# Performance work log

Measured on AMD Instinct MI355X. Metric: run time of the kernel, lower is better.

Reference implementation:

```python
import jax, jax.numpy as jnp
import numpy as np

N_HEADS = 16
D_EMBED = 1024
N_CROSS = 768
D_HEAD = D_EMBED // N_HEADS


def setup_inputs() -> dict:
    key = jax.random.key(0)
    ks = jax.random.split(key, 10)
    B, S = 2, 2048
    x = jax.random.normal(ks[0], (B, S, D_EMBED), dtype=jnp.float32)
    context = jax.random.normal(ks[1], (B, S, N_CROSS), dtype=jnp.float32)
    sq = 1.0 / np.sqrt(D_EMBED)
    sc = 1.0 / np.sqrt(N_CROSS)
    Wq = jax.random.normal(ks[2], (D_EMBED, D_EMBED), dtype=jnp.float32) * sq
    bq = jnp.zeros((D_EMBED,), dtype=jnp.float32)
    Wk = jax.random.normal(ks[3], (N_CROSS, D_EMBED), dtype=jnp.float32) * sc
    bk = jnp.zeros((D_EMBED,), dtype=jnp.float32)
    Wv = jax.random.normal(ks[4], (N_CROSS, D_EMBED), dtype=jnp.float32) * sc
    bv = jnp.zeros((D_EMBED,), dtype=jnp.float32)
    Wo = jax.random.normal(ks[5], (D_EMBED, D_EMBED), dtype=jnp.float32) * sq
    bo = jnp.zeros((D_EMBED,), dtype=jnp.float32)
    return {"x": x, "context": context, "Wq": Wq, "bq": bq, "Wk": Wk, "bk": bk,
            "Wv": Wv, "bv": bv, "Wo": Wo, "bo": bo}


def reference(x, context, Wq, bq, Wk, bk, Wv, bv, Wo, bo):
    B, S, _ = x.shape

    def split_heads(t):  # [B,S,E] -> [B,H,S,Dh]
        return t.reshape(B, S, N_HEADS, D_HEAD).transpose(0, 2, 1, 3)

    q = split_heads(x @ Wq + bq)
    k = split_heads(context @ Wk + bk)
    v = split_heads(context @ Wv + bv)

    scale = 1.0 / np.sqrt(D_HEAD)
    scores = jnp.einsum('bhqd,bhkd->bhqk', q, k) * scale
    attn = jax.nn.softmax(scores, axis=-1)
    out = jnp.einsum('bhqk,bhkd->bhqd', attn, v)
    out = out.transpose(0, 2, 1, 3).reshape(B, S, D_EMBED)
    return out @ Wo + bo
```

## Files before the change

### kernel.cpp

```cpp
#include <hip/hip_runtime.h>
#include <math.h>


namespace {

typedef short bfr __attribute__((ext_vector_type(8)));
typedef short s4v __attribute__((ext_vector_type(4)));
typedef unsigned u4v __attribute__((ext_vector_type(4)));
typedef float accf __attribute__((ext_vector_type(16)));

#define MFMA32(a, b, c) __builtin_amdgcn_mfma_f32_32x32x16_bf16(a, b, c, 0, 0, 0)

__device__ inline short f2bf(float f) {
    unsigned u = __float_as_uint(f);
    u += 0x7fffu + ((u >> 16) & 1u);
    return (short)(u >> 16);
}
__device__ inline float bf2f(short s) {
    return __uint_as_float(((unsigned)(unsigned short)s) << 16);
}
__device__ inline float fexp2(float x) { return __builtin_amdgcn_exp2f(x); }
__device__ inline accf zero16() {
    accf z;
#pragma unroll
    for (int i = 0; i < 16; ++i) z[i] = 0.f;
    return z;
}
__device__ inline void dma16(const void* g, void* l) {
    __builtin_amdgcn_global_load_lds(
        (const __attribute__((address_space(1))) void*)g,
        (__attribute__((address_space(3))) void*)l, 16, 0, 0);
}

__global__ __launch_bounds__(256) void prep(
    const float* __restrict__ x, const float* __restrict__ ctx,
    short* __restrict__ xb, short* __restrict__ cb,
    const float* __restrict__ Wq, const float* __restrict__ Wk,
    const float* __restrict__ Wv, const float* __restrict__ Wo,
    short* __restrict__ Wqt, short* __restrict__ Wkt,
    short* __restrict__ Wvt, short* __restrict__ Wot) {
    __shared__ short t[64][68];
    const int bx = blockIdx.x;
    if (bx < 7168) {
        int i = bx * 256 + threadIdx.x;
        if (i < 1048576) {
            float4 v = ((const float4*)x)[i];
            s4v p = {f2bf(v.x), f2bf(v.y), f2bf(v.z), f2bf(v.w)};
            ((s4v*)xb)[i] = p;
        } else {
            int j = i - 1048576;
            float4 v = ((const float4*)ctx)[j];
            s4v p = {f2bf(v.x), f2bf(v.y), f2bf(v.z), f2bf(v.w)};
            ((s4v*)cb)[j] = p;
        }
        return;
    }
    const int idx = bx - 7168;
    const int z = idx >> 8, gy = (idx >> 4) & 15, gx = idx & 15;
    const float* W;
    short* Wt;
    int K;
    switch (z) {
        case 0: W = Wq; Wt = Wqt; K = 1024; break;
        case 1: W = Wk; Wt = Wkt; K = 768; break;
        case 2: W = Wv; Wt = Wvt; K = 768; break;
        default: W = Wo; Wt = Wot; K = 1024; break;
    }
    const int k0 = gy * 64;
    if (k0 >= K) return;
    const int tid = threadIdx.x;
    const int n0 = gx * 64;
    const int kr = tid >> 4, nc = (tid & 15) * 4;
#pragma unroll
    for (int rep = 0; rep < 4; ++rep) {
        int k = kr + rep * 16;
        float4 v = *(const float4*)&W[(size_t)(k0 + k) * 1024 + n0 + nc];
        t[nc + 0][k] = f2bf(v.x);
        t[nc + 1][k] = f2bf(v.y);
        t[nc + 2][k] = f2bf(v.z);
        t[nc + 3][k] = f2bf(v.w);
    }
    __syncthreads();
    const int nr = tid >> 4, kc = (tid & 15) * 4;
#pragma unroll
    for (int rep = 0; rep < 4; ++rep) {
        int n = nr + rep * 16;
        s4v p = {t[n][kc], t[n][kc + 1], t[n][kc + 2], t[n][kc + 3]};
        *(s4v*)&Wt[(size_t)(n0 + n) * K + k0 + kc] = p;
    }
}

__global__ __launch_bounds__(512, 6) void gemm_qkv(
    const short* __restrict__ xb, const short* __restrict__ cb,
    const short* __restrict__ Wqt, const short* __restrict__ Wkt,
    const short* __restrict__ Wvt, const float* __restrict__ bq,
    const float* __restrict__ bk, const float* __restrict__ bv,
    short* __restrict__ Qf, short* __restrict__ Kf, short* __restrict__ Vt,
    float qscale) {
    const int bid = blockIdx.x;
    const int z = bid >> 8;
    const int local = bid & 255;
    const short* A  = (z == 0) ? xb : cb;
    const short* Bt = (z == 0) ? Wqt : ((z == 1) ? Wkt : Wvt);
    const float* bias = (z == 0) ? bq : ((z == 1) ? bk : bv);
    const int K = (z == 0) ? 1024 : 768;
    const int NIT = K / 32;
    const float scale = (z == 0) ? qscale : 1.f;
    short* out = (z == 0) ? Qf : ((z == 1) ? Kf : Vt);

    __shared__ short As[12288];
    __shared__ short Bs[12288];
    const int t = threadIdx.x, lane = t & 63, w = t >> 6;
    const int lm = lane & 31, h2 = lane >> 5;
    const int wm = w & 1, wn = w >> 1;
    const int m0 = (local & 31) * 128, n0 = (local >> 5) * 128;

    const int st = t ^ ((t >> 3) & 7);
    const int srow = st >> 2, scol = (st & 3) * 8;
    const short* ga = A + (size_t)(m0 + srow) * K + scol;
    const short* gb = Bt + (size_t)(n0 + srow) * K + scol;

    const int xorv = (lm >> 1) & 7;
    const int rA0 = wm * 64 + lm, rB0 = wn * 32 + lm;

    accf acc[2] = {zero16(), zero16()};

    dma16(ga, &As[w * 512]);
    dma16(gb, &Bs[w * 512]);
    __builtin_amdgcn_sched_barrier(0);
    dma16(ga + 32, &As[4096 + w * 512]);
    dma16(gb + 32, &Bs[4096 + w * 512]);
    __builtin_amdgcn_sched_barrier(0);

    int buf = 0;
#pragma unroll 1
    for (int it = 0; it < NIT; ++it) {
        __builtin_amdgcn_sched_barrier(0);
        asm volatile("s_waitcnt vmcnt(2)" ::: "memory");
        __builtin_amdgcn_s_barrier();
        __builtin_amdgcn_sched_barrier(0);
        {
            const int nx = (it + 2 >= NIT) ? (it + 2 - NIT) : (it + 2);
            const int nb = (buf + 2 >= 3) ? (buf - 1) : (buf + 2);
            dma16(ga + nx * 32, &As[nb * 4096 + w * 512]);
            dma16(gb + nx * 32, &Bs[nb * 4096 + w * 512]);
        }
        const short* bA = &As[buf * 4096];
        const short* bB = &Bs[buf * 4096];
#pragma unroll
        for (int kk8 = 0; kk8 < 4; kk8 += 2) {
            bfr a0 = *(const bfr*)&bA[((rA0 * 4 + h2 + kk8) ^ xorv) * 8];
            bfr a1 = *(const bfr*)&bA[(((rA0 + 32) * 4 + h2 + kk8) ^ xorv) * 8];
            bfr b0 = *(const bfr*)&bB[((rB0 * 4 + h2 + kk8) ^ xorv) * 8];
            acc[0] = MFMA32(a0, b0, acc[0]);
            acc[1] = MFMA32(a1, b0, acc[1]);
        }
        buf = (buf + 1 == 3) ? 0 : buf + 1;
    }
    asm volatile("s_waitcnt vmcnt(0)" ::: "memory");
    __builtin_amdgcn_sched_barrier(0);

    const int n = n0 + wn * 32 + lm;
    const float bn = bias[n];
    const int hh = n >> 6, dd = n & 63;
#pragma unroll
    for (int mt = 0; mt < 2; ++mt) {
        const int mbase = m0 + wm * 64 + mt * 32 + 4 * h2;
        if (z != 2) {
            const int cb2 = (dd >> 4) * 512 + ((dd >> 3) & 1) * 256 + (dd & 7);
#pragma unroll
            for (int r = 0; r < 16; ++r) {
                const int m = mbase + (r & 3) + 8 * (r >> 2);
                const int bb = m >> 11, q = m & 2047;
                float v = (acc[mt][r] + bn) * scale;
                out[((size_t)((bb * 16 + hh) * 64 + (q >> 5))) * 2048 +
                    cb2 + (q & 31) * 8] = f2bf(v);
            }
        } else {
            const int dblk = dd >> 5, lmv = dd & 31;
#pragma unroll
            for (int g = 0; g < 4; ++g) {
                const int m = mbase + 8 * g;
                const int bb = m >> 11, s = m & 2047;
                const int kvt = s >> 6, kc = (s >> 4) & 3;
                const int h2v = (s >> 3) & 1, j0 = s & 7;
                s4v pq = {f2bf(acc[mt][4 * g + 0] + bn),
                          f2bf(acc[mt][4 * g + 1] + bn),
                          f2bf(acc[mt][4 * g + 2] + bn),
                          f2bf(acc[mt][4 * g + 3] + bn)};
                *(s4v*)(out +
                        ((size_t)(((bb * 16 + hh) * 32 + kvt) * 2 + dblk)) * 2048 +
                        kc * 512 + h2v * 256 + lmv * 8 + j0) = pq;
            }
        }
    }
}

__global__ __launch_bounds__(512) void gemm_out(
    const short* __restrict__ p0, const short* __restrict__ p1,
    const float* __restrict__ lsum, const short* __restrict__ Bt,
    const float* __restrict__ bias, float* __restrict__ out) {
    constexpr int K = 1024, NIT = 32;
    __shared__ short As[8192];
    __shared__ short Bs[8192];
    const int t = threadIdx.x, lane = t & 63, w = t >> 6;
    const int lm = lane & 31, h2 = lane >> 5;
    const int wm = w & 1, wn = w >> 1;
    const int bid = blockIdx.x;
    const int m0 = (bid & 31) * 128, n0 = (bid >> 5) * 128;

    const int st = t ^ ((t >> 3) & 7);
    const int srow = st >> 2, scol = (st & 3) * 8;
    const int gm = m0 + srow;
    const int b = gm >> 11, q = gm & 2047;
    const short* pa0 = p0 + (size_t)gm * 1024 + scol;
    const short* pa1 = p1 + (size_t)gm * 1024 + scol;
    const short* gb = Bt + (size_t)(n0 + srow) * K + scol;

    float inv[16];
#pragma unroll
    for (int h = 0; h < 16; ++h) {
        float l0 = lsum[((size_t)b * 16 + h) * 2048 + q];
        float l1 = lsum[((size_t)(2 + b) * 16 + h) * 2048 + q];
        inv[h] = 1.f / (l0 + l1);
    }

    const int xorv = (lm >> 1) & 7;
    const int rA0 = wm * 64 + lm, rB0 = wn * 32 + lm;

    accf acc[2] = {zero16(), zero16()};

    dma16(gb, &Bs[w * 512]);
    {
        bfr v0 = *(const bfr*)pa0;
        bfr v1 = *(const bfr*)pa1;
        const float iv = inv[0];
        bfr pk;
#pragma unroll
        for (int j = 0; j < 8; ++j)
            pk[j] = f2bf((bf2f(v0[j]) + bf2f(v1[j])) * iv);
        *(bfr*)&As[t * 8] = pk;
    }

#pragma unroll 1
    for (int it = 0; it < NIT; ++it) {
        const int p = it & 1;
        __syncthreads();
        bfr v0, v1;
        const bool nxt = (it + 1 < NIT);
        if (nxt) {
            const int ktn = (it + 1) * 32;
            dma16(gb + ktn, &Bs[(1 - p) * 4096 + w * 512]);
            v0 = *(const bfr*)(pa0 + ktn);
            v1 = *(const bfr*)(pa1 + ktn);
        }
        const short* bA = &As[p * 4096];
        const short* bB = &Bs[p * 4096];
#pragma unroll
        for (int kk8 = 0; kk8 < 4; kk8 += 2) {
            bfr a0 = *(const bfr*)&bA[((rA0 * 4 + h2 + kk8) ^ xorv) * 8];
            bfr a1 = *(const bfr*)&bA[(((rA0 + 32) * 4 + h2 + kk8) ^ xorv) * 8];
            bfr b0 = *(const bfr*)&bB[((rB0 * 4 + h2 + kk8) ^ xorv) * 8];
            acc[0] = MFMA32(a0, b0, acc[0]);
            acc[1] = MFMA32(a1, b0, acc[1]);
        }
        if (nxt) {
            const float iv = inv[(it + 1) >> 1];
            bfr pk;
#pragma unroll
            for (int j = 0; j < 8; ++j)
                pk[j] = f2bf((bf2f(v0[j]) + bf2f(v1[j])) * iv);
            *(bfr*)&As[(1 - p) * 4096 + t * 8] = pk;
        }
    }

    const int n = n0 + wn * 32 + lm;
    const float bn = bias[n];
#pragma unroll
    for (int mt = 0; mt < 2; ++mt) {
        const int mbase = m0 + wm * 64 + mt * 32 + 4 * h2;
#pragma unroll
        for (int r = 0; r < 16; ++r) {
            const int m = mbase + (r & 3) + 8 * (r >> 2);
            out[(size_t)m * 1024 + n] = acc[mt][r] + bn;
        }
    }
}

__global__ __launch_bounds__(256, 3) void attn(
    const short* __restrict__ Qf, const short* __restrict__ Kf,
    const short* __restrict__ Vt, short* __restrict__ part,
    float* __restrict__ lsum) {
    __shared__ short smem[16384];
    const int bid = blockIdx.x;
    const int hidx = bid & 31, qs = bid >> 5;
    const int split = qs & 1, qb = qs >> 1;
    const int b = hidx >> 4, h = hidx & 15;
    const int lane = threadIdx.x & 63, wv = threadIdx.x >> 6;
    const int lm = lane & 31, h2 = lane >> 5;
    const bool hb = h2 != 0;
    const int q0 = qb * 128 + wv * 32;

    const short* qbase =
        Qf + ((size_t)(hidx * 64 + (q0 >> 5))) * 2048 + lane * 8;
    bfr qf[4];
#pragma unroll
    for (int kc = 0; kc < 4; ++kc) qf[kc] = *(const bfr*)(qbase + kc * 512);

    const short* khead = Kf + (size_t)hidx * 131072 + split * 65536;
    const short* vhead = Vt + (size_t)hidx * 131072 + split * 65536;
    const short* gsrc =
        ((wv < 2) ? (khead + wv * 2048) : (vhead + (wv - 2) * 2048)) + lane * 8;

#pragma unroll
    for (int i = 0; i < 4; ++i)
        dma16(gsrc + i * 512, &smem[wv * 2048 + i * 512]);

    accf oa0 = zero16(), oa1 = zero16();
    float la0 = 0.f, la1 = 0.f;

#pragma unroll 1
    for (int it = 0; it < 16; ++it) {
        const int p = it & 1;
        __syncthreads();
        if (it + 1 < 16) {
            const short* gn = gsrc + (size_t)(it + 1) * 4096;
            short* ln = &smem[(1 - p) * 8192 + wv * 2048];
#pragma unroll
            for (int i = 0; i < 4; ++i) dma16(gn + i * 512, ln + i * 512);
        }
        const short* kb = &smem[p * 8192];
        bfr kf0[4], kf1[4], vf0[4], vf1[4];
#pragma unroll
        for (int kc = 0; kc < 4; ++kc) {
            kf0[kc] = *(const bfr*)&kb[kc * 512 + lane * 8];
            kf1[kc] = *(const bfr*)&kb[2048 + kc * 512 + lane * 8];
            vf0[kc] = *(const bfr*)&kb[4096 + kc * 512 + lane * 8];
            vf1[kc] = *(const bfr*)&kb[6144 + kc * 512 + lane * 8];
        }
        accf s0 = zero16(), s1 = zero16();
#pragma unroll
        for (int kc = 0; kc < 4; ++kc) {
            s0 = MFMA32(kf0[kc], qf[kc], s0);
            s1 = MFMA32(kf1[kc], qf[kc], s1);
        }

#pragma unroll
        for (int i = 0; i < 16; ++i) s0[i] = fexp2(s0[i]);
#pragma unroll
        for (int i = 0; i < 16; ++i) s1[i] = fexp2(s1[i]);
#pragma unroll
        for (int i = 0; i < 16; ++i) {
            if (i & 1) la1 += s0[i] + s1[i];
            else       la0 += s0[i] + s1[i];
        }

        bfr pb[4];
#pragma unroll
        for (int kc = 0; kc < 4; ++kc) {
            const accf& s = (kc < 2) ? s0 : s1;
            const int base = 8 * (kc & 1);
            unsigned Lw0 = __builtin_amdgcn_perm(__float_as_uint(s[base + 1]),
                                                 __float_as_uint(s[base + 0]),
                                                 0x07060302u);
            unsigned Lw1 = __builtin_amdgcn_perm(__float_as_uint(s[base + 3]),
                                                 __float_as_uint(s[base + 2]),
                                                 0x07060302u);
            unsigned Hw0 = __builtin_amdgcn_perm(__float_as_uint(s[base + 5]),
                                                 __float_as_uint(s[base + 4]),
                                                 0x07060302u);
            unsigned Hw1 = __builtin_amdgcn_perm(__float_as_uint(s[base + 7]),
                                                 __float_as_uint(s[base + 6]),
                                                 0x07060302u);
            unsigned c0 = hb ? Lw0 : Hw0;
            unsigned c1 = hb ? Lw1 : Hw1;
            unsigned r0 = (unsigned)__shfl_xor((int)c0, 32);
            unsigned r1 = (unsigned)__shfl_xor((int)c1, 32);
            u4v pw = {hb ? r0 : Lw0, hb ? r1 : Lw1,
                      hb ? Hw0 : r0, hb ? Hw1 : r1};
            pb[kc] = __builtin_bit_cast(bfr, pw);
        }

#pragma unroll
        for (int kc = 0; kc < 4; ++kc) {
            oa0 = MFMA32(vf0[kc], pb[kc], oa0);
            oa1 = MFMA32(vf1[kc], pb[kc], oa1);
        }
    }

    float ls = la0 + la1;
    ls += __shfl_xor(ls, 32);
    if (!hb) lsum[((size_t)(split * 2 + b) * 16 + h) * 2048 + q0 + lm] = ls;

    short* orow = part + (size_t)split * 4194304 +
                  (size_t)(b * 2048 + q0 + lm) * 1024 + h * 64;
#pragma unroll
    for (int dt = 0; dt < 2; ++dt) {
        const accf& oa = dt ? oa1 : oa0;
#pragma unroll
        for (int g = 0; g < 4; ++g) {
            const int d0 = dt * 32 + 4 * h2 + 8 * g;
            s4v p = {f2bf(oa[4 * g + 0]), f2bf(oa[4 * g + 1]),
                     f2bf(oa[4 * g + 2]), f2bf(oa[4 * g + 3])};
            *(s4v*)(orow + d0) = p;
        }
    }
}

}

extern "C" void kernel_launch(void* const* d_in, const int* in_sizes, int n_in,
                              void* d_out, int out_size, void* d_ws,
                              size_t ws_size, hipStream_t stream) {
    const float* x   = (const float*)d_in[0];
    const float* ctx = (const float*)d_in[1];
    const float* Wq  = (const float*)d_in[2];
    const float* bq  = (const float*)d_in[3];
    const float* Wk  = (const float*)d_in[4];
    const float* bk  = (const float*)d_in[5];
    const float* Wv  = (const float*)d_in[6];
    const float* bv  = (const float*)d_in[7];
    const float* Wo  = (const float*)d_in[8];
    const float* bo  = (const float*)d_in[9];

    short* xb  = (short*)d_ws;
    short* cb  = xb + (size_t)4096 * 1024;
    short* Wqt = cb + (size_t)4096 * 768;
    short* Wkt = Wqt + (size_t)1024 * 1024;
    short* Wvt = Wkt + (size_t)1024 * 768;
    short* Wot = Wvt + (size_t)1024 * 768;
    short* Qf  = Wot + (size_t)1024 * 1024;
    short* Kf  = Qf + (size_t)4096 * 1024;
    short* Vt  = Kf + (size_t)4096 * 1024;
    short* p0  = Vt + (size_t)4096 * 1024;
    short* p1  = p0 + (size_t)4096 * 1024;
    float* lsum = (float*)(p1 + (size_t)4096 * 1024);

    prep<<<8192, 256, 0, stream>>>(x, ctx, xb, cb, Wq, Wk, Wv, Wo,
                                   Wqt, Wkt, Wvt, Wot);

    const float qscale = 0.125f * 1.44269504088896f;
    gemm_qkv<<<768, 512, 0, stream>>>(xb, cb, Wqt, Wkt, Wvt,
                                      bq, bk, bv, Qf, Kf, Vt, qscale);

    attn<<<1024, 256, 0, stream>>>(Qf, Kf, Vt, p0, lsum);

    gemm_out<<<256, 512, 0, stream>>>(p0, p1, lsum, Wot, bo, (float*)d_out);
}
```

Baseline: 208.2 us.

## Split split-KV combine into separate kernel and triple-buffer DMA output GEMM

The normalisation and merge of the two split-KV attention partials moves out of the output-projection GEMM into a standalone elementwise kernel that writes the normalised bf16 result back into p0. The output GEMM then loads both A and B tiles by direct DMA into a three-stage shared-memory ring, waiting with explicit vmcnt and barriers instead of doing register-side conversion in the loop. This aims to hide global latency better in the GEMM, at the cost of an extra kernel launch and an extra read/write pass over the 8MB partial buffer. Past the end of K, the prefetch wraps around and loads redundant tiles.

```diff
diff --git a/kernel.cpp b/kernel.cpp
--- a/kernel.cpp
+++ b/kernel.cpp
@@ -196,13 +196,32 @@
     }
 }
 
-__global__ __launch_bounds__(512) void gemm_out(
-    const short* __restrict__ p0, const short* __restrict__ p1,
-    const float* __restrict__ lsum, const short* __restrict__ Bt,
+__global__ __launch_bounds__(256) void combine(
+    short* __restrict__ p0, const short* __restrict__ p1,
+    const float* __restrict__ lsum) {
+    const int i = blockIdx.x * 256 + threadIdx.x;
+    const size_t gi = (size_t)i * 8;
+    const int row = (int)(gi >> 10), col = (int)(gi & 1023);
+    const int h = col >> 6;
+    const int b = row >> 11, q = row & 2047;
+    const float l0 = lsum[((size_t)b * 16 + h) * 2048 + q];
+    const float l1 = lsum[((size_t)(2 + b) * 16 + h) * 2048 + q];
+    const float iv = 1.f / (l0 + l1);
+    bfr v0 = *(const bfr*)(p0 + gi);
+    bfr v1 = *(const bfr*)(p1 + gi);
+    bfr pk;
+#pragma unroll
+    for (int j = 0; j < 8; ++j)
+        pk[j] = f2bf((bf2f(v0[j]) + bf2f(v1[j])) * iv);
+    *(bfr*)(p0 + gi) = pk;
+}
+
+__global__ __launch_bounds__(512, 6) void gemm_o(
+    const short* __restrict__ Af, const short* __restrict__ Bt,
     const float* __restrict__ bias, float* __restrict__ out) {
     constexpr int K = 1024, NIT = 32;
-    __shared__ short As[8192];
-    __shared__ short Bs[8192];
+    __shared__ short As[12288];
+    __shared__ short Bs[12288];
     const int t = threadIdx.x, lane = t & 63, w = t >> 6;
     const int lm = lane & 31, h2 = lane >> 5;
     const int wm = w & 1, wn = w >> 1;
@@ -211,51 +230,36 @@
 
     const int st = t ^ ((t >> 3) & 7);
     const int srow = st >> 2, scol = (st & 3) * 8;
-    const int gm = m0 + srow;
-    const int b = gm >> 11, q = gm & 2047;
-    const short* pa0 = p0 + (size_t)gm * 1024 + scol;
-    const short* pa1 = p1 + (size_t)gm * 1024 + scol;
+    const short* ga = Af + (size_t)(m0 + srow) * K + scol;
     const short* gb = Bt + (size_t)(n0 + srow) * K + scol;
-
-    float inv[16];
-#pragma unroll
-    for (int h = 0; h < 16; ++h) {
-        float l0 = lsum[((size_t)b * 16 + h) * 2048 + q];
-        float l1 = lsum[((size_t)(2 + b) * 16 + h) * 2048 + q];
-        inv[h] = 1.f / (l0 + l1);
-    }
 
     const int xorv = (lm >> 1) & 7;
     const int rA0 = wm * 64 + lm, rB0 = wn * 32 + lm;
 
     accf acc[2] = {zero16(), zero16()};
 
+    dma16(ga, &As[w * 512]);
     dma16(gb, &Bs[w * 512]);
-    {
-        bfr v0 = *(const bfr*)pa0;
-        bfr v1 = *(const bfr*)pa1;
-        const float iv = inv[0];
-        bfr pk;
-#pragma unroll
-        for (int j = 0; j < 8; ++j)
-            pk[j] = f2bf((bf2f(v0[j]) + bf2f(v1[j])) * iv);
-        *(bfr*)&As[t * 8] = pk;
-    }
-
+    __builtin_amdgcn_sched_barrier(0);
+    dma16(ga + 32, &As[4096 + w * 512]);
+    dma16(gb + 32, &Bs[4096 + w * 512]);
+    __builtin_amdgcn_sched_barrier(0);
+
+    int buf = 0;
 #pragma unroll 1
     for (int it = 0; it < NIT; ++it) {
-        const int p = it & 1;
-        __syncthreads();
-        bfr v0, v1;
-        const bool nxt = (it + 1 < NIT);
-        if (nxt) {
-            const int ktn = (it + 1) * 32;
-            dma16(gb + ktn, &Bs[(1 - p) * 4096 + w * 512]);
-            v0 = *(const bfr*)(pa0 + ktn);
-            v1 = *(const bfr*)(pa1 + ktn);
-        }
-        const short* bA = &As[p * 4096];
-        const short* bB = &Bs[p * 4096];
+        __builtin_amdgcn_sched_barrier(0);
+        asm volatile("s_waitcnt vmcnt(2)" ::: "memory");
+        __builtin_amdgcn_s_barrier();
+        __builtin_amdgcn_sched_barrier(0);
+        {
+            const int nx = (it + 2 >= NIT) ? (it + 2 - NIT) : (it + 2);
+            const int nb = (buf + 2 >= 3) ? (buf - 1) : (buf + 2);
+            dma16(ga + nx * 32, &As[nb * 4096 + w * 512]);
+            dma16(gb + nx * 32, &Bs[nb * 4096 + w * 512]);
+        }
+        const short* bA = &As[buf * 4096];
+        const short* bB = &Bs[buf * 4096];
 #pragma unroll
         for (int kk8 = 0; kk8 < 4; kk8 += 2) {
             bfr a0 = *(const bfr*)&bA[((rA0 * 4 + h2 + kk8) ^ xorv) * 8];
@@ -264,15 +268,10 @@
             acc[0] = MFMA32(a0, b0, acc[0]);
             acc[1] = MFMA32(a1, b0, acc[1]);
         }
-        if (nxt) {
-            const float iv = inv[(it + 1) >> 1];
-            bfr pk;
-#pragma unroll
-            for (int j = 0; j < 8; ++j)
-                pk[j] = f2bf((bf2f(v0[j]) + bf2f(v1[j])) * iv);
-            *(bfr*)&As[(1 - p) * 4096 + t * 8] = pk;
-        }
-    }
+        buf = (buf + 1 == 3) ? 0 : buf + 1;
+    }
+    asm volatile("s_waitcnt vmcnt(0)" ::: "memory");
+    __builtin_amdgcn_sched_barrier(0);
 
     const int n = n0 + wn * 32 + lm;
     const float bn = bias[n];
@@ -445,5 +444,7 @@
 
     attn<<<1024, 256, 0, stream>>>(Qf, Kf, Vt, p0, lsum);
 
-    gemm_out<<<256, 512, 0, stream>>>(p0, p1, lsum, Wot, bo, (float*)d_out);
-}
+    combine<<<2048, 256, 0, stream>>>(p0, p1, lsum);
+
+    gemm_o<<<256, 512, 0, stream>>>(p0, Wot, bo, (float*)d_out);
+}
```

New measurement: 203.5 us. 2.2% less time.
